# Kernel tuning notes

Measured on AMD Instinct MI355X. Metric: run time of the kernel, lower is better.

The kernel has to match this reference:

```python
import jax, jax.numpy as jnp
import numpy as np

B, T, W, E, H, EMB, NVOCAB, WIN = 256, 200, 200, 768, 256, 32, 201, 8


def setup_inputs() -> dict:
    key = jax.random.key(0)
    ks = jax.random.split(key, 12)
    s = 0.05
    inputs = jax.random.normal(ks[0], (B, T, E), jnp.float32)
    full_word_embeddings = jax.random.normal(ks[1], (B, W, E), jnp.float32)
    lengths = jax.random.randint(ks[2], (B,), T // 2, T + 1)
    fix = jax.random.randint(ks[3], (B, T), 1, NVOCAB)
    fix_seq = jnp.where(jnp.arange(T)[None, :] < lengths[:, None], fix, 0)
    emb_table = (jax.random.normal(ks[4], (NVOCAB, EMB)) * s).at[0].set(0.0)  # padding_idx=0
    W_ih = jax.random.normal(ks[5], (3 * H, E + EMB)) * s  # torch GRU layout, gates r,z,n
    W_hh = jax.random.normal(ks[6], (3 * H, H)) * s
    b_ih = jax.random.normal(ks[7], (3 * H,)) * s
    b_hh = jax.random.normal(ks[8], (3 * H,)) * s
    W_out = jax.random.normal(ks[9], (E, H)) * s  # output_layer: Linear(H, E)
    b_out = jnp.zeros((E,), jnp.float32)
    W_dur = jax.random.normal(ks[10], (1, H)) * s  # duration_layer: Linear(H, 1)
    b_dur = jnp.zeros((1,), jnp.float32)
    return {"inputs": inputs, "fix_seq": fix_seq, "full_word_embeddings": full_word_embeddings,
            "lengths": lengths, "expert_id": 0, "emb_table": emb_table,
            "W_ih": W_ih, "b_ih": b_ih, "W_hh": W_hh, "b_hh": b_hh,
            "W_out": W_out, "b_out": b_out, "W_dur": W_dur, "b_dur": b_dur}


def _gru(x, W_ih, b_ih, W_hh, b_hh, h_dim):
    # x: [B,T,I]. Precompute input projections once, scan over time.
    xg = jnp.einsum('bti,gi->btg', x, W_ih) + b_ih  # [B,T,3H]

    def step(h, xg_t):
        hg = h @ W_hh.T + b_hh
        xr, xz, xn = jnp.split(xg_t, 3, axis=-1)
        hr, hz, hn = jnp.split(hg, 3, axis=-1)
        r = jax.nn.sigmoid(xr + hr)
        z = jax.nn.sigmoid(xz + hz)
        n = jnp.tanh(xn + r * hn)
        h_new = (1.0 - z) * n + z * h
        return h_new, h_new

    h0 = jnp.zeros((x.shape[0], h_dim), x.dtype)
    _, outs = jax.lax.scan(step, h0, jnp.swapaxes(xg, 0, 1))
    return jnp.swapaxes(outs, 0, 1)  # [B,T,H]


def reference(inputs, fix_seq, full_word_embeddings, lengths, expert_id,
              emb_table, W_ih, b_ih, W_hh, b_hh, W_out, b_out, W_dur, b_dur):
    del expert_id  # weights of the selected expert are passed directly
    valid_mask = fix_seq != 0
    scan_emb = emb_table[fix_seq]  # [B,T,32]
    rnn_in = jnp.concatenate([inputs, scan_emb], axis=-1)
    outputs = _gru(rnn_in, W_ih, b_ih, W_hh, b_hh, W_hh.shape[1])  # [B,T,H]
    # pad_packed_sequence zeros outputs beyond each sequence length
    tmask = jnp.arange(outputs.shape[1])[None, :] < lengths[:, None]
    outputs = outputs * tmask[..., None].astype(outputs.dtype)
    # dot attention: proj then scores against word embeddings
    proj = outputs @ W_out.T + b_out  # [B,T,E]
    logits = jnp.einsum('bte,bwe->btw', proj, full_word_embeddings)
    # saccade window mask around current fixation position
    wpos = jnp.arange(full_word_embeddings.shape[1])[None, None, :]
    dist = jnp.abs(wpos - fix_seq[..., None])
    sacc = (dist <= WIN) & valid_mask[..., None]
    logits = jnp.where(sacc, logits, -1e9)
    word_mask = jnp.sum(jnp.abs(full_word_embeddings), axis=-1) != 0
    logits = jnp.where(word_mask[:, None, :], logits, -1e9)
    dur_pred = (outputs @ W_dur.T + b_dur)[..., 0]  # [B,T]
    return logits, dur_pred
```

## Files before the change

kernel.cpp:

```cpp
#include <hip/hip_runtime.h>
#include <hip/hip_bf16.h>

typedef __attribute__((ext_vector_type(8))) short bf16x8;
typedef __attribute__((ext_vector_type(4))) float f32x4;
typedef __attribute__((ext_vector_type(4))) int   i32x4;

#define NB 256
#define NT 200
#define NW 200
#define NE 768
#define NH 256
#define NEMB 32
#define KIN 800
#define G3H 768
#define MROWS 51200

__device__ __forceinline__ float bf2f(unsigned short h) {
    return __uint_as_float(((unsigned)h) << 16);
}
__device__ __forceinline__ unsigned short f2bf(float f) {
    unsigned u = __float_as_uint(f);
    u += 0x7fff + ((u >> 16) & 1);
    return (unsigned short)(u >> 16);
}
__device__ __forceinline__ float sigm(float x) { return 1.0f / (1.0f + __expf(-x)); }
__device__ __forceinline__ float tanh_fast(float x) {
    float e = __expf(2.0f * x);
    return 1.0f - 2.0f / (e + 1.0f);
}

#if __has_builtin(__builtin_amdgcn_sdot4)
__device__ __forceinline__ int SDOT4(int a, int b, int c) {
    return __builtin_amdgcn_sdot4(a, b, c, false);
}
#else
__device__ __forceinline__ int SDOT4(int a, int b, int c) {
    #pragma unroll
    for (int j = 0; j < 4; j++)
        c += (int)(signed char)(a >> (8 * j)) * (int)(signed char)(b >> (8 * j));
    return c;
}
#endif

__device__ __forceinline__ void gload16(const void* g, void* l) {
    __builtin_amdgcn_global_load_lds((const __attribute__((address_space(1))) unsigned int*)g,
                                     (__attribute__((address_space(3))) unsigned int*)l,
                                     16, 0, 0);
}

__global__ void prep1(const float* __restrict__ inputs, const int* __restrict__ fix_seq,
                      const float* __restrict__ emb, const float* __restrict__ Wih,
                      const float* __restrict__ Wout, const float* __restrict__ bih,
                      const float* __restrict__ bhh,
                      unsigned short* __restrict__ Abf, unsigned short* __restrict__ Wihbf,
                      unsigned short* __restrict__ WoutTbf, float* __restrict__ biasC) {
    const long gid0 = (long)blockIdx.x * blockDim.x + threadIdx.x;
    if (gid0 < G3H) biasC[gid0] = bih[gid0] + (gid0 < 512 ? bhh[gid0] : 0.0f);
    const long NA = (long)MROWS * 100;
    const long NWU = 768L * 100;
    const long NOU = 256L * 96;
    const long total = NA + NWU + NOU;
    for (long u = gid0; u < total; u += (long)gridDim.x * blockDim.x) {
        bf16x8 v;
        unsigned short* dst;
        if (u < NA) {
            long row = u / 100;
            int c8 = (int)(u % 100) * 8;
            const float* s;
            if (c8 < NE) {
                s = inputs + row * NE + c8;
            } else {
                int fx = fix_seq[row];
                s = emb + (long)fx * NEMB + (c8 - NE);
            }
            #pragma unroll
            for (int j = 0; j < 8; j++) v[j] = (short)f2bf(s[j]);
            dst = Abf + row * KIN + c8;
        } else if (u < NA + NWU) {
            long u2 = u - NA;
            long row = u2 / 100;
            int c8 = (int)(u2 % 100) * 8;
            const float* s = Wih + row * KIN + c8;
            #pragma unroll
            for (int j = 0; j < 8; j++) v[j] = (short)f2bf(s[j]);
            dst = Wihbf + row * KIN + c8;
        } else {
            long u3 = u - NA - NWU;
            long row = u3 / 96;
            int c8 = (int)(u3 % 96) * 8;
            #pragma unroll
            for (int j = 0; j < 8; j++)
                v[j] = (short)f2bf(Wout[(long)(c8 + j) * NH + row]);
            dst = WoutTbf + row * NE + c8;
        }
        *(bf16x8*)dst = v;
    }
}

__global__ __launch_bounds__(256)
void gemm_bt128(const unsigned short* __restrict__ A,
                const unsigned short* __restrict__ Bw,
                const float* __restrict__ bias,
                unsigned short* __restrict__ Out,
                int M, int N, int K) {
    __shared__ unsigned short As[2][128 * 32];
    __shared__ unsigned short Bs[2][128 * 32];
    const int bid = (int)((blockIdx.x & 7) * (gridDim.x >> 3) + (blockIdx.x >> 3));
    const int nblk = N >> 7;
    const int m0 = (bid / nblk) << 7;
    const int n0 = (bid % nblk) << 7;
    const int tid = threadIdx.x;
    const int lane = tid & 63;
    const int wave = tid >> 6;
    const int wm = (wave >> 1) << 6;
    const int wn = (wave & 1) << 6;
    const int nk = K >> 5;

    const int srow = tid >> 2;
    const int sseg = (tid & 3) << 4;
    const char* gA0 = (const char*)(A + (long)(m0 + srow) * K) + sseg;
    const char* gA1 = (const char*)(A + (long)(m0 + 64 + srow) * K) + sseg;
    const char* gB0 = (const char*)(Bw + (long)(n0 + srow) * K) + sseg;
    const char* gB1 = (const char*)(Bw + (long)(n0 + 64 + srow) * K) + sseg;
    const int lofs = wave * 1024;

    f32x4 acc[4][4] = {};

    gload16(gA0, (char*)As[0] + lofs);
    gload16(gA1, (char*)As[0] + 4096 + lofs);
    gload16(gB0, (char*)Bs[0] + lofs);
    gload16(gB1, (char*)Bs[0] + 4096 + lofs);

    int cur = 0;
    for (int kt = 0; kt < nk; kt++) {
        if (kt + 1 < nk) {
            gload16(gA0 + (kt + 1) * 64, (char*)As[cur ^ 1] + lofs);
            gload16(gA1 + (kt + 1) * 64, (char*)As[cur ^ 1] + 4096 + lofs);
            gload16(gB0 + (kt + 1) * 64, (char*)Bs[cur ^ 1] + lofs);
            gload16(gB1 + (kt + 1) * 64, (char*)Bs[cur ^ 1] + 4096 + lofs);
            asm volatile("s_waitcnt vmcnt(4)" ::: "memory");
        } else {
            asm volatile("s_waitcnt vmcnt(0)" ::: "memory");
        }
        __builtin_amdgcn_sched_barrier(0);
        __builtin_amdgcn_s_barrier();
        __builtin_amdgcn_sched_barrier(0);
        bf16x8 af[4], bfr[4];
        #pragma unroll
        for (int mi = 0; mi < 4; mi++)
            af[mi] = *(const bf16x8*)((const char*)As[cur] +
                        (wm + mi * 16 + (lane & 15)) * 64 + ((lane >> 4) << 4));
        #pragma unroll
        for (int ni = 0; ni < 4; ni++)
            bfr[ni] = *(const bf16x8*)((const char*)Bs[cur] +
                        (wn + ni * 16 + (lane & 15)) * 64 + ((lane >> 4) << 4));
        #pragma unroll
        for (int mi = 0; mi < 4; mi++)
            #pragma unroll
            for (int ni = 0; ni < 4; ni++)
                acc[mi][ni] = __builtin_amdgcn_mfma_f32_16x16x32_bf16(
                                  af[mi], bfr[ni], acc[mi][ni], 0, 0, 0);
        asm volatile("s_waitcnt lgkmcnt(0)" ::: "memory");
        __builtin_amdgcn_sched_barrier(0);
        __builtin_amdgcn_s_barrier();
        __builtin_amdgcn_sched_barrier(0);
        cur ^= 1;
    }
    #pragma unroll
    for (int ni = 0; ni < 4; ni++) {
        const int col = n0 + wn + ni * 16 + (lane & 15);
        const float bv = bias[col];
        #pragma unroll
        for (int mi = 0; mi < 4; mi++) {
            const int row = m0 + wm + mi * 16 + ((lane >> 4) << 2);
            #pragma unroll
            for (int r = 0; r < 4; r++)
                Out[(long)(row + r) * N + col] = f2bf(acc[mi][ni][r] + bv);
        }
    }
}

__global__ __launch_bounds__(256)
void gemmG_f32(const float* __restrict__ fwe,
               const unsigned short* __restrict__ BwT,
               const float* __restrict__ bout,
               unsigned short* __restrict__ G,
               unsigned char* __restrict__ wmask,
               float* __restrict__ dvec) {
    __shared__ unsigned short As[128 * 32];
    __shared__ unsigned short Bs[128 * 32];
    __shared__ float Bo[G3H];
    const int bid = (int)((blockIdx.x & 7) * (gridDim.x >> 3) + (blockIdx.x >> 3));
    const int m0 = (bid >> 1) << 7;
    const int n0 = (bid & 1) << 7;
    const int tid = threadIdx.x;
    const int lane = tid & 63;
    const int wave = tid >> 6;
    const int wm = (wave >> 1) << 6;
    const int wn = (wave & 1) << 6;

    const int srow = tid >> 2;
    const int sseg = (tid & 3) << 4;
    const char* gB0 = (const char*)(BwT + (long)(n0 + srow) * NE) + sseg;
    const char* gB1 = (const char*)(BwT + (long)(n0 + 64 + srow) * NE) + sseg;
    char* lB0 = (char*)Bs + wave * 1024;
    char* lB1 = (char*)Bs + 4096 + wave * 1024;

    const int arow = tid >> 1;
    const int akh = tid & 1;
    const float* aptr = fwe + (long)(m0 + arow) * NE + akh * 16;
    char* la = (char*)As + arow * 64 + akh * 32;

    for (int i = tid; i < G3H; i += 256) Bo[i] = bout[i];

    float4 fa0 = *(const float4*)(aptr);
    float4 fa1 = *(const float4*)(aptr + 4);
    float4 fa2 = *(const float4*)(aptr + 8);
    float4 fa3 = *(const float4*)(aptr + 12);

    f32x4 acc[4][4] = {};
    float asum = 0.0f, vdot = 0.0f;

    __syncthreads();

    for (int kt = 0; kt < 24; kt++) {
        __syncthreads();
        gload16(gB0 + kt * 64, lB0);
        gload16(gB1 + kt * 64, lB1);
        const float* bo = Bo + kt * 32 + akh * 16;
        const float4 b0 = *(const float4*)(bo);
        const float4 b1 = *(const float4*)(bo + 4);
        const float4 b2 = *(const float4*)(bo + 8);
        const float4 b3 = *(const float4*)(bo + 12);
        asum += fabsf(fa0.x) + fabsf(fa0.y) + fabsf(fa0.z) + fabsf(fa0.w)
              + fabsf(fa1.x) + fabsf(fa1.y) + fabsf(fa1.z) + fabsf(fa1.w)
              + fabsf(fa2.x) + fabsf(fa2.y) + fabsf(fa2.z) + fabsf(fa2.w)
              + fabsf(fa3.x) + fabsf(fa3.y) + fabsf(fa3.z) + fabsf(fa3.w);
        vdot += fa0.x * b0.x + fa0.y * b0.y + fa0.z * b0.z + fa0.w * b0.w
              + fa1.x * b1.x + fa1.y * b1.y + fa1.z * b1.z + fa1.w * b1.w
              + fa2.x * b2.x + fa2.y * b2.y + fa2.z * b2.z + fa2.w * b2.w
              + fa3.x * b3.x + fa3.y * b3.y + fa3.z * b3.z + fa3.w * b3.w;
        bf16x8 v0, v1;
        v0[0] = (short)f2bf(fa0.x); v0[1] = (short)f2bf(fa0.y);
        v0[2] = (short)f2bf(fa0.z); v0[3] = (short)f2bf(fa0.w);
        v0[4] = (short)f2bf(fa1.x); v0[5] = (short)f2bf(fa1.y);
        v0[6] = (short)f2bf(fa1.z); v0[7] = (short)f2bf(fa1.w);
        v1[0] = (short)f2bf(fa2.x); v1[1] = (short)f2bf(fa2.y);
        v1[2] = (short)f2bf(fa2.z); v1[3] = (short)f2bf(fa2.w);
        v1[4] = (short)f2bf(fa3.x); v1[5] = (short)f2bf(fa3.y);
        v1[6] = (short)f2bf(fa3.z); v1[7] = (short)f2bf(fa3.w);
        *(bf16x8*)la = v0;
        *(bf16x8*)(la + 16) = v1;
        asm volatile("s_waitcnt vmcnt(0)" ::: "memory");
        __syncthreads();
        if (kt + 1 < 24) {
            const float* ap = aptr + (kt + 1) * 32;
            fa0 = *(const float4*)(ap);
            fa1 = *(const float4*)(ap + 4);
            fa2 = *(const float4*)(ap + 8);
            fa3 = *(const float4*)(ap + 12);
        }
        bf16x8 af[4], bfr[4];
        #pragma unroll
        for (int mi = 0; mi < 4; mi++)
            af[mi] = *(const bf16x8*)((const char*)As +
                        (wm + mi * 16 + (lane & 15)) * 64 + ((lane >> 4) << 4));
        #pragma unroll
        for (int ni = 0; ni < 4; ni++)
            bfr[ni] = *(const bf16x8*)((const char*)Bs +
                        (wn + ni * 16 + (lane & 15)) * 64 + ((lane >> 4) << 4));
        #pragma unroll
        for (int mi = 0; mi < 4; mi++)
            #pragma unroll
            for (int ni = 0; ni < 4; ni++)
                acc[mi][ni] = __builtin_amdgcn_mfma_f32_16x16x32_bf16(
                                  af[mi], bfr[ni], acc[mi][ni], 0, 0, 0);
    }
    asum += __shfl_xor(asum, 1);
    vdot += __shfl_xor(vdot, 1);
    if (akh == 0) {
        wmask[m0 + arow] = (asum != 0.0f) ? 1 : 0;
        dvec[m0 + arow] = vdot;
    }
    #pragma unroll
    for (int ni = 0; ni < 4; ni++) {
        const int col = n0 + wn + ni * 16 + (lane & 15);
        #pragma unroll
        for (int mi = 0; mi < 4; mi++) {
            const int row = m0 + wm + mi * 16 + ((lane >> 4) << 2);
            #pragma unroll
            for (int r = 0; r < 4; r++)
                G[(long)(row + r) * NH + col] = f2bf(acc[mi][ni][r]);
        }
    }
}

__global__ __launch_bounds__(512, 2)
__attribute__((amdgpu_waves_per_eu(2, 2)))
void gru_scan(const unsigned short* __restrict__ xg,
              const float* __restrict__ Whh,
              const float* __restrict__ bhh,
              const int* __restrict__ lengths,
              unsigned short* __restrict__ hout) {
    __shared__ __align__(16) unsigned char h8[2][256];
    const int tid = threadIdx.x;
    const int lane = tid & 63;
    const int wave = tid >> 6;
    const int b = blockIdx.x;
    const int col = wave * 32 + (lane & 31);
    const int kh = lane >> 5;

    int W[3][32];
    #pragma unroll
    for (int g = 0; g < 3; g++) {
        const float* wr = Whh + (long)(g * 256 + col) * NH + kh * 128;
        #pragma unroll
        for (int d = 0; d < 32; d++) {
            const float4 f = *(const float4*)(wr + d * 4);
            unsigned pack = 0;
            #pragma unroll
            for (int j = 0; j < 4; j++) {
                const float fv = j == 0 ? f.x : j == 1 ? f.y : j == 2 ? f.z : f.w;
                int wq = (int)rintf(fv * 400.0f);
                wq = wq > 127 ? 127 : (wq < -127 ? -127 : wq);
                pack |= ((unsigned)(wq & 0xff)) << (8 * j);
            }
            W[g][d] = (int)pack;
        }
    }
    const float bhn = bhh[512 + col];
    const int len = lengths[b];
    if (tid < 128) ((unsigned*)h8)[tid] = 0u;

    const unsigned short* xrow = xg + (long)b * NT * G3H;
    unsigned short xv0 = xrow[col], xv1 = xrow[256 + col], xv2 = xrow[512 + col];
    float hp = 0.0f;
    const float ISC = 1.0f / (400.0f * 127.0f);
    const bool wlo = (lane < 32);

    asm volatile("s_waitcnt lgkmcnt(0)" ::: "memory");
    __builtin_amdgcn_sched_barrier(0);
    __builtin_amdgcn_s_barrier();
    __builtin_amdgcn_sched_barrier(0);

    for (int t = 0; t < NT; t++) {
        const unsigned char* hb = h8[(t + 1) & 1] + kh * 128;
        int p0a = 0, p0b = 0, p1a = 0, p1b = 0, p2a = 0, p2b = 0;
        #pragma unroll
        for (int r = 0; r < 8; r++) {
            const i32x4 hv = *(const i32x4*)(hb + r * 16);
            p0a = SDOT4(hv[0], W[0][r * 4 + 0], p0a);
            p1a = SDOT4(hv[0], W[1][r * 4 + 0], p1a);
            p2a = SDOT4(hv[0], W[2][r * 4 + 0], p2a);
            p0b = SDOT4(hv[1], W[0][r * 4 + 1], p0b);
            p1b = SDOT4(hv[1], W[1][r * 4 + 1], p1b);
            p2b = SDOT4(hv[1], W[2][r * 4 + 1], p2b);
            p0a = SDOT4(hv[2], W[0][r * 4 + 2], p0a);
            p1a = SDOT4(hv[2], W[1][r * 4 + 2], p1a);
            p2a = SDOT4(hv[2], W[2][r * 4 + 2], p2a);
            p0b = SDOT4(hv[3], W[0][r * 4 + 3], p0b);
            p1b = SDOT4(hv[3], W[1][r * 4 + 3], p1b);
            p2b = SDOT4(hv[3], W[2][r * 4 + 3], p2b);
        }
        int p0 = p0a + p0b, p1 = p1a + p1b, p2 = p2a + p2b;
        p0 += __shfl_xor(p0, 32);
        p1 += __shfl_xor(p1, 32);
        p2 += __shfl_xor(p2, 32);
        const float r = sigm(bf2f(xv0) + (float)p0 * ISC);
        const float z = sigm(bf2f(xv1) + (float)p1 * ISC);
        const float n = tanh_fast(bf2f(xv2) + r * ((float)p2 * ISC + bhn));
        hp = (1.0f - z) * n + z * hp;
        if (wlo) {
            h8[t & 1][col] = (unsigned char)((int)rintf(hp * 127.0f) & 0xff);
            hout[((long)b * NT + t) * NH + col] = (t < len) ? f2bf(hp) : (unsigned short)0;
        }
        if (t + 1 < NT) {
            const unsigned short* xn = xrow + (long)(t + 1) * G3H;
            xv0 = xn[col]; xv1 = xn[256 + col]; xv2 = xn[512 + col];
        }
        asm volatile("s_waitcnt lgkmcnt(0)" ::: "memory");
        __builtin_amdgcn_sched_barrier(0);
        __builtin_amdgcn_s_barrier();
        __builtin_amdgcn_sched_barrier(0);
    }
}

__global__ __launch_bounds__(256)
void logits_dur(const unsigned short* __restrict__ Hrow,
                const unsigned short* __restrict__ G,
                const int* __restrict__ fix_seq,
                const unsigned char* __restrict__ wmask,
                const float* __restrict__ dvec,
                const float* __restrict__ Wdur, const float* __restrict__ bdur,
                float* __restrict__ out) {
    __shared__ float dots[4][20];
    const int wv = threadIdx.x >> 6;
    const int gwave = (int)blockIdx.x * 4 + wv;
    const int lane = threadIdx.x & 63;
    const int l16 = lane & 15;
    const int grp = lane >> 4;
    const int b = gwave / NT;

    const unsigned short* hp = Hrow + (long)gwave * NH + l16 * 16;
    const bf16x8 h0 = *(const bf16x8*)hp;
    const bf16x8 h1 = *(const bf16x8*)(hp + 8);
    float hf[16];
    #pragma unroll
    for (int j = 0; j < 8; j++) { hf[j] = bf2f((unsigned short)h0[j]);
                                  hf[8 + j] = bf2f((unsigned short)h1[j]); }

    const int fix = fix_seq[gwave];
    const int wbase = fix - 8;

    if (fix != 0) {
        #pragma unroll
        for (int it = 0; it < 5; it++) {
            const int wi = it * 4 + grp;
            int w = wbase + wi;
            w = w < 0 ? 0 : (w > NW - 1 ? NW - 1 : w);
            const unsigned short* gp = G + ((long)b * NW + w) * NH + l16 * 16;
            const bf16x8 g0 = *(const bf16x8*)gp;
            const bf16x8 g1 = *(const bf16x8*)(gp + 8);
            float p = 0.0f;
            #pragma unroll
            for (int j = 0; j < 8; j++) {
                p += hf[j] * bf2f((unsigned short)g0[j]);
                p += hf[8 + j] * bf2f((unsigned short)g1[j]);
            }
            p += __shfl_xor(p, 1); p += __shfl_xor(p, 2);
            p += __shfl_xor(p, 4); p += __shfl_xor(p, 8);
            if (l16 == 0 && wi < 17) dots[wv][wi] = p;
        }
    }
    float pd = 0.0f;
    #pragma unroll
    for (int j = 0; j < 16; j++) pd += hf[j] * Wdur[l16 * 16 + j];
    pd += __shfl_xor(pd, 1); pd += __shfl_xor(pd, 2);
    pd += __shfl_xor(pd, 4); pd += __shfl_xor(pd, 8);
    if (lane == 0) out[(long)NB * NT * NW + gwave] = pd + bdur[0];

    __syncthreads();

    if (lane < 50) {
        float4 o;
        #pragma unroll
        for (int c = 0; c < 4; c++) {
            const int w = lane * 4 + c;
            const int wi = w - wbase;
            const int wic = wi < 0 ? 0 : (wi > 16 ? 16 : wi);
            const bool ok = (fix != 0) && ((unsigned)wi < 17u) && (wmask[b * NW + w] != 0);
            const float val = dots[wv][wic] + dvec[b * NW + w];
            ((float*)&o)[c] = ok ? val : -1e9f;
        }
        *(float4*)(out + (long)gwave * NW + lane * 4) = o;
    }
}

extern "C" void kernel_launch(void* const* d_in, const int* in_sizes, int n_in,
                              void* d_out, int out_size, void* d_ws, size_t ws_size,
                              hipStream_t stream) {
    (void)in_sizes; (void)n_in; (void)out_size; (void)ws_size;
    const float* inputs  = (const float*)d_in[0];
    const int*   fix_seq = (const int*)d_in[1];
    const float* fwe     = (const float*)d_in[2];
    const int*   lengths = (const int*)d_in[3];
    const float* emb     = (const float*)d_in[5];
    const float* Wih     = (const float*)d_in[6];
    const float* bih     = (const float*)d_in[7];
    const float* Whh     = (const float*)d_in[8];
    const float* bhh     = (const float*)d_in[9];
    const float* Wout    = (const float*)d_in[10];
    const float* bout    = (const float*)d_in[11];
    const float* Wdur    = (const float*)d_in[12];
    const float* bdur    = (const float*)d_in[13];
    float* out = (float*)d_out;

    char* ws = (char*)d_ws;
    unsigned short* Abf     = (unsigned short*)(ws);
    unsigned short* xgbf    = (unsigned short*)(ws + 81920000);
    unsigned short* hout    = (unsigned short*)(ws + 160563200);
    unsigned short* Wihbf   = (unsigned short*)(ws + 186777600);
    unsigned short* WoutTbf = (unsigned short*)(ws + 188006400);
    unsigned char*  wmask   = (unsigned char*)(ws + 188399616);
    float*          biasC   = (float*)(ws + 188450816);
    float*          dvec    = (float*)(ws + 188453888);
    unsigned short* Gbf     = Abf;

    prep1<<<2048, 256, 0, stream>>>(inputs, fix_seq, emb, Wih, Wout, bih, bhh,
                                    Abf, Wihbf, WoutTbf, biasC);
    gemm_bt128<<<400 * 6, 256, 0, stream>>>(Abf, Wihbf, biasC, xgbf, MROWS, G3H, KIN);
    gemmG_f32<<<800, 256, 0, stream>>>(fwe, WoutTbf, bout, Gbf, wmask, dvec);
    gru_scan<<<256, 512, 0, stream>>>(xgbf, Whh, bhh, lengths, hout);
    logits_dur<<<12800, 256, 0, stream>>>(hout, Gbf, fix_seq, wmask, dvec, Wdur, bdur, out);
}
```

Baseline: 499.9 us.

## Widen gemmG tile to cover full N so fp32 A rows load once

The word-embedding projection GEMM now uses 512-thread blocks whose 128x256 tile spans the whole N=256 output, instead of two 128x128 blocks per M tile. Each fp32 row of full_word_embeddings is read, converted to bf16, and reduced for the word mask and bias dot only once rather than twice. This halves redundant global A traffic and conversion work. In exchange the grid has 400 larger blocks with more shared memory each, and the L2-friendly block swizzle is dropped.

```diff
diff --git a/kernel.cpp b/kernel.cpp
--- a/kernel.cpp
+++ b/kernel.cpp
@@ -180,7 +180,7 @@
     }
 }
 
-__global__ __launch_bounds__(256)
+__global__ __launch_bounds__(512)
 void gemmG_f32(const float* __restrict__ fwe,
                const unsigned short* __restrict__ BwT,
                const float* __restrict__ bout,
@@ -188,35 +188,30 @@
                unsigned char* __restrict__ wmask,
                float* __restrict__ dvec) {
     __shared__ unsigned short As[128 * 32];
-    __shared__ unsigned short Bs[128 * 32];
+    __shared__ unsigned short Bs[256 * 32];
     __shared__ float Bo[G3H];
-    const int bid = (int)((blockIdx.x & 7) * (gridDim.x >> 3) + (blockIdx.x >> 3));
-    const int m0 = (bid >> 1) << 7;
-    const int n0 = (bid & 1) << 7;
+    const int m0 = (int)blockIdx.x << 7;
     const int tid = threadIdx.x;
     const int lane = tid & 63;
     const int wave = tid >> 6;
-    const int wm = (wave >> 1) << 6;
-    const int wn = (wave & 1) << 6;
-
-    const int srow = tid >> 2;
+    const int wm = (wave >> 2) << 6;
+    const int wn = (wave & 3) << 6;
+
+    const int arow = tid >> 2;
+    const int akq = tid & 3;
+    const float* aptr = fwe + (long)(m0 + arow) * NE + akq * 8;
+    char* la = (char*)As + arow * 64 + akq * 16;
+
     const int sseg = (tid & 3) << 4;
-    const char* gB0 = (const char*)(BwT + (long)(n0 + srow) * NE) + sseg;
-    const char* gB1 = (const char*)(BwT + (long)(n0 + 64 + srow) * NE) + sseg;
-    char* lB0 = (char*)Bs + wave * 1024;
-    char* lB1 = (char*)Bs + 4096 + wave * 1024;
-
-    const int arow = tid >> 1;
-    const int akh = tid & 1;
-    const float* aptr = fwe + (long)(m0 + arow) * NE + akh * 16;
-    char* la = (char*)As + arow * 64 + akh * 32;
-
-    for (int i = tid; i < G3H; i += 256) Bo[i] = bout[i];
+    const char* gBa = (const char*)(BwT + (long)arow * NE) + sseg;
+    const char* gBb = (const char*)(BwT + (long)(128 + arow) * NE) + sseg;
+    char* lBa = (char*)Bs + wave * 1024;
+    char* lBb = (char*)Bs + 8192 + wave * 1024;
+
+    for (int i = tid; i < G3H; i += 512) Bo[i] = bout[i];
 
     float4 fa0 = *(const float4*)(aptr);
     float4 fa1 = *(const float4*)(aptr + 4);
-    float4 fa2 = *(const float4*)(aptr + 8);
-    float4 fa3 = *(const float4*)(aptr + 12);
 
     f32x4 acc[4][4] = {};
     float asum = 0.0f, vdot = 0.0f;
@@ -225,40 +220,27 @@
 
     for (int kt = 0; kt < 24; kt++) {
         __syncthreads();
-        gload16(gB0 + kt * 64, lB0);
-        gload16(gB1 + kt * 64, lB1);
-        const float* bo = Bo + kt * 32 + akh * 16;
+        gload16(gBa + kt * 64, lBa);
+        gload16(gBb + kt * 64, lBb);
+        const float* bo = Bo + kt * 32 + akq * 8;
         const float4 b0 = *(const float4*)(bo);
         const float4 b1 = *(const float4*)(bo + 4);
-        const float4 b2 = *(const float4*)(bo + 8);
-        const float4 b3 = *(const float4*)(bo + 12);
         asum += fabsf(fa0.x) + fabsf(fa0.y) + fabsf(fa0.z) + fabsf(fa0.w)
-              + fabsf(fa1.x) + fabsf(fa1.y) + fabsf(fa1.z) + fabsf(fa1.w)
-              + fabsf(fa2.x) + fabsf(fa2.y) + fabsf(fa2.z) + fabsf(fa2.w)
-              + fabsf(fa3.x) + fabsf(fa3.y) + fabsf(fa3.z) + fabsf(fa3.w);
+              + fabsf(fa1.x) + fabsf(fa1.y) + fabsf(fa1.z) + fabsf(fa1.w);
         vdot += fa0.x * b0.x + fa0.y * b0.y + fa0.z * b0.z + fa0.w * b0.w
-              + fa1.x * b1.x + fa1.y * b1.y + fa1.z * b1.z + fa1.w * b1.w
-              + fa2.x * b2.x + fa2.y * b2.y + fa2.z * b2.z + fa2.w * b2.w
-              + fa3.x * b3.x + fa3.y * b3.y + fa3.z * b3.z + fa3.w * b3.w;
-        bf16x8 v0, v1;
-        v0[0] = (short)f2bf(fa0.x); v0[1] = (short)f2bf(fa0.y);
-        v0[2] = (short)f2bf(fa0.z); v0[3] = (short)f2bf(fa0.w);
-        v0[4] = (short)f2bf(fa1.x); v0[5] = (short)f2bf(fa1.y);
-        v0[6] = (short)f2bf(fa1.z); v0[7] = (short)f2bf(fa1.w);
-        v1[0] = (short)f2bf(fa2.x); v1[1] = (short)f2bf(fa2.y);
-        v1[2] = (short)f2bf(fa2.z); v1[3] = (short)f2bf(fa2.w);
-        v1[4] = (short)f2bf(fa3.x); v1[5] = (short)f2bf(fa3.y);
-        v1[6] = (short)f2bf(fa3.z); v1[7] = (short)f2bf(fa3.w);
-        *(bf16x8*)la = v0;
-        *(bf16x8*)(la + 16) = v1;
+              + fa1.x * b1.x + fa1.y * b1.y + fa1.z * b1.z + fa1.w * b1.w;
+        bf16x8 v;
+        v[0] = (short)f2bf(fa0.x); v[1] = (short)f2bf(fa0.y);
+        v[2] = (short)f2bf(fa0.z); v[3] = (short)f2bf(fa0.w);
+        v[4] = (short)f2bf(fa1.x); v[5] = (short)f2bf(fa1.y);
+        v[6] = (short)f2bf(fa1.z); v[7] = (short)f2bf(fa1.w);
+        *(bf16x8*)la = v;
         asm volatile("s_waitcnt vmcnt(0)" ::: "memory");
         __syncthreads();
         if (kt + 1 < 24) {
             const float* ap = aptr + (kt + 1) * 32;
             fa0 = *(const float4*)(ap);
             fa1 = *(const float4*)(ap + 4);
-            fa2 = *(const float4*)(ap + 8);
-            fa3 = *(const float4*)(ap + 12);
         }
         bf16x8 af[4], bfr[4];
         #pragma unroll
@@ -276,15 +258,15 @@
                 acc[mi][ni] = __builtin_amdgcn_mfma_f32_16x16x32_bf16(
                                   af[mi], bfr[ni], acc[mi][ni], 0, 0, 0);
     }
-    asum += __shfl_xor(asum, 1);
-    vdot += __shfl_xor(vdot, 1);
-    if (akh == 0) {
+    asum += __shfl_xor(asum, 1);  asum += __shfl_xor(asum, 2);
+    vdot += __shfl_xor(vdot, 1);  vdot += __shfl_xor(vdot, 2);
+    if (akq == 0) {
         wmask[m0 + arow] = (asum != 0.0f) ? 1 : 0;
         dvec[m0 + arow] = vdot;
     }
     #pragma unroll
     for (int ni = 0; ni < 4; ni++) {
-        const int col = n0 + wn + ni * 16 + (lane & 15);
+        const int col = wn + ni * 16 + (lane & 15);
         #pragma unroll
         for (int mi = 0; mi < 4; mi++) {
             const int row = m0 + wm + mi * 16 + ((lane >> 4) << 2);
@@ -489,7 +471,7 @@
     prep1<<<2048, 256, 0, stream>>>(inputs, fix_seq, emb, Wih, Wout, bih, bhh,
                                     Abf, Wihbf, WoutTbf, biasC);
     gemm_bt128<<<400 * 6, 256, 0, stream>>>(Abf, Wihbf, biasC, xgbf, MROWS, G3H, KIN);
-    gemmG_f32<<<800, 256, 0, stream>>>(fwe, WoutTbf, bout, Gbf, wmask, dvec);
+    gemmG_f32<<<400, 512, 0, stream>>>(fwe, WoutTbf, bout, Gbf, wmask, dvec);
     gru_scan<<<256, 512, 0, stream>>>(xgbf, Whh, bhh, lengths, hout);
     logits_dur<<<12800, 256, 0, stream>>>(hout, Gbf, fix_seq, wmask, dvec, Wdur, bdur, out);
 }
```

Measured after the change: 463.4 us. 7.3% less time.
